# Kernel tuning notes

Measured on AMD Instinct MI355X. Metric: run time of the kernel, lower is better.

Reference implementation:

```python
import jax, jax.numpy as jnp
import numpy as np

N_NODES = 100000
HIDDEN = 256
HALF = HIDDEN // 2
N_EDGES = 1000000


def setup_inputs() -> dict:
    key = jax.random.key(0)
    k1, k2 = jax.random.split(key)
    x = jax.random.normal(k1, (N_NODES, HIDDEN), dtype=jnp.float32)
    edge_label_index = jax.random.randint(k2, (2, N_EDGES), 0, N_NODES, dtype=jnp.int64)
    return {"x": x, "edge_label_index": edge_label_index}


def reference(x, edge_label_index):
    # Gather source-half features for src nodes and target-half for dst nodes,
    # per-edge dot product, sigmoid. Output shape [E, 1] as in the torch module.
    src = x[edge_label_index[0], :HALF]          # [E, HALF]
    dst = x[edge_label_index[1], HALF:]          # [E, HALF]
    logits = jnp.einsum('ed,ed->e', src, dst)    # per-edge dot
    return jax.nn.sigmoid(logits).reshape(-1, 1)
```

## Files before the change

kernel.cpp:

```cpp
#include <hip/hip_runtime.h>
#include <hip/hip_bf16.h>
#include <math.h>


#define HIDDEN 256
#define HALF   128

__global__ __launch_bounds__(256) void decoder_src_tgt_kernel(
    const float* __restrict__ x,
    const int* __restrict__ eidx,
    float* __restrict__ out,
    int n_edges)
{
    int tid  = blockIdx.x * blockDim.x + threadIdx.x;
    int edge = tid >> 5;
    int lane = tid & 31;
    if (edge >= n_edges) return;

    int s = eidx[edge];
    int d = eidx[n_edges + edge];

    const float4* sp = (const float4*)(x + (size_t)s * HIDDEN) + lane;
    const float4* dp = (const float4*)(x + (size_t)d * HIDDEN + HALF) + lane;

    float4 a = *sp;
    float4 b = *dp;
    float acc = a.x * b.x + a.y * b.y + a.z * b.z + a.w * b.w;

    #pragma unroll
    for (int off = 16; off > 0; off >>= 1)
        acc += __shfl_down(acc, off, 32);

    if (lane == 0) {
        out[edge] = 1.0f / (1.0f + __expf(-acc));
    }
}

extern "C" void kernel_launch(void* const* d_in, const int* in_sizes, int n_in,
                              void* d_out, int out_size, void* d_ws, size_t ws_size,
                              hipStream_t stream)
{
    const float* x    = (const float*)d_in[0];
    const int*   eidx = (const int*)d_in[1];
    float*       out  = (float*)d_out;

    int n_edges = out_size;

    const int threads = 256;
    const int edges_per_block = threads / 32;
    int blocks = (n_edges + edges_per_block - 1) / edges_per_block;

    decoder_src_tgt_kernel<<<blocks, threads, 0, stream>>>(x, eidx, out, n_edges);
}
```

Before: 265.4 us.

## Convert node features to fp16 in workspace and gather half-width rows

```diff
diff --git a/kernel.cpp b/kernel.cpp
--- a/kernel.cpp
+++ b/kernel.cpp
@@ -6,7 +6,59 @@
 #define HIDDEN 256
 #define HALF   128
 
-__global__ __launch_bounds__(256) void decoder_src_tgt_kernel(
+typedef _Float16 half8 __attribute__((ext_vector_type(8)));
+
+__global__ __launch_bounds__(256) void cvt_fp16_kernel(
+    const float* __restrict__ x, _Float16* __restrict__ y, int n8)
+{
+    int i = blockIdx.x * blockDim.x + threadIdx.x;
+    if (i >= n8) return;
+    const float4* p = (const float4*)x + (size_t)2 * i;
+    float4 a = p[0];
+    float4 b = p[1];
+    half8 h;
+    h[0] = (_Float16)a.x; h[1] = (_Float16)a.y;
+    h[2] = (_Float16)a.z; h[3] = (_Float16)a.w;
+    h[4] = (_Float16)b.x; h[5] = (_Float16)b.y;
+    h[6] = (_Float16)b.z; h[7] = (_Float16)b.w;
+    ((half8*)y)[i] = h;
+}
+
+__global__ __launch_bounds__(256) void decoder_fp16_kernel(
+    const _Float16* __restrict__ y,
+    const int* __restrict__ eidx,
+    float* __restrict__ out,
+    int n_edges)
+{
+    int tid  = blockIdx.x * blockDim.x + threadIdx.x;
+    int edge = tid >> 4;
+    int lane = tid & 15;
+    if (edge >= n_edges) return;
+
+    int s = eidx[edge];
+    int d = eidx[n_edges + edge];
+
+    const half8* sp = (const half8*)(y + (size_t)s * HIDDEN) + lane;
+    const half8* dp = (const half8*)(y + (size_t)d * HIDDEN + HALF) + lane;
+
+    half8 a = *sp;
+    half8 b = *dp;
+
+    float acc = 0.f;
+    #pragma unroll
+    for (int j = 0; j < 8; ++j)
+        acc += (float)a[j] * (float)b[j];
+
+    #pragma unroll
+    for (int off = 8; off > 0; off >>= 1)
+        acc += __shfl_down(acc, off, 16);
+
+    if (lane == 0) {
+        out[edge] = 1.0f / (1.0f + __expf(-acc));
+    }
+}
+
+__global__ __launch_bounds__(256) void decoder_fp32_kernel(
     const float* __restrict__ x,
     const int* __restrict__ eidx,
     float* __restrict__ out,
@@ -44,11 +96,24 @@
     const int*   eidx = (const int*)d_in[1];
     float*       out  = (float*)d_out;
 
-    int n_edges = out_size;
+    int n_edges  = out_size;
+    int n_elems  = in_sizes[0];
+    size_t need  = (size_t)n_elems * 2;
 
-    const int threads = 256;
-    const int edges_per_block = threads / 32;
-    int blocks = (n_edges + edges_per_block - 1) / edges_per_block;
+    if (ws_size >= need) {
+        _Float16* y = (_Float16*)d_ws;
 
-    decoder_src_tgt_kernel<<<blocks, threads, 0, stream>>>(x, eidx, out, n_edges);
+        int n8 = n_elems / 8;
+        cvt_fp16_kernel<<<(n8 + 255) / 256, 256, 0, stream>>>(x, y, n8);
+
+        const int threads = 256;
+        const int epb = threads / 16;
+        int blocks = (n_edges + epb - 1) / epb;
+        decoder_fp16_kernel<<<blocks, threads, 0, stream>>>(y, eidx, out, n_edges);
+    } else {
+        const int threads = 256;
+        const int epb = threads / 32;
+        int blocks = (n_edges + epb - 1) / epb;
+        decoder_fp32_kernel<<<blocks, threads, 0, stream>>>(x, eidx, out, n_edges);
+    }
 }
```

Measured after the change: 225.0 us. 1.18x faster.
